# Performance work log

Measured on AMD Instinct MI355X. Metric: run time of the kernel, lower is better.

Reference implementation:

```python
import jax, jax.numpy as jnp
import numpy as np

B, S, D = 2, 1024, 2048
MLP_RATIO = 4
N_LAYERS = 2
H = D * MLP_RATIO
EPS = 1e-5


def _act_quant(x):
    # BitNet b1.58: per-token int8 absmax quantization over last dim
    scale = 127.0 / jnp.clip(jnp.max(jnp.abs(x), axis=-1, keepdims=True), EPS, None)
    return jnp.clip(jnp.round(x * scale), -128.0, 127.0) / scale


def _weight_quant(w):
    # BitNet b1.58: per-tensor ternary quantization with mean-abs scale
    scale = 1.0 / jnp.clip(jnp.mean(jnp.abs(w)), EPS, None)
    return jnp.clip(jnp.round(w * scale), -1.0, 1.0) / scale


def _ste(v, quant_fn):
    # straight-through estimator: forward quantized, backward identity
    return v + jax.lax.stop_gradient(quant_fn(v) - v)


def bit_linear(x, w, b):
    # x: [B,S,in], w: [out,in], b: [out]
    xq = _ste(x, _act_quant)
    wq = _ste(w, _weight_quant)
    return jnp.einsum('bsi,oi->bso', xq, wq) + b


def setup_inputs() -> dict:
    key = jax.random.key(0)
    ks = jax.random.split(key, 16)
    inp = {
        'x': jax.random.normal(ks[0], (B, S, D), jnp.float32),
        'y': jax.random.normal(ks[1], (B, S, D), jnp.float32),
        'z': jax.random.normal(ks[2], (B, S, D), jnp.float32),
        'focus_mask': jax.random.uniform(ks[3], (B, S, 1), jnp.float32),
        'w_in': jax.random.normal(ks[4], (D, 3 * D), jnp.float32) * 0.02,
        'b_in': jnp.zeros((D,), jnp.float32),
        'fc1_w': jax.random.normal(ks[5], (N_LAYERS, H, D), jnp.float32) * 0.02,
        'fc1_b': jnp.zeros((N_LAYERS, H), jnp.float32),
        'fc2_w': jax.random.normal(ks[6], (N_LAYERS, D, H), jnp.float32) * 0.02,
        'fc2_b': jnp.zeros((N_LAYERS, D), jnp.float32),
        'w_out': jax.random.normal(ks[7], (D, D), jnp.float32) * 0.02,
        'b_out': jnp.zeros((D,), jnp.float32),
    }
    return inp


def reference(x, y, z, focus_mask, w_in, b_in, fc1_w, fc1_b, fc2_w, fc2_b, w_out, b_out):
    h = bit_linear(jnp.concatenate([x, y, z], axis=-1), w_in, b_in)
    for l in range(N_LAYERS):
        u = jax.nn.gelu(bit_linear(h, fc1_w[l], fc1_b[l]), approximate=False)
        h = h + bit_linear(u, fc2_w[l], fc2_b[l])
    delta = bit_linear(h, w_out, b_out)
    return y + focus_mask * delta
```

## Files before the change

### kernel.cpp

```cpp
#include <hip/hip_runtime.h>

#define EPSQ 1e-5f

typedef int i32x4 __attribute__((ext_vector_type(4)));
typedef float f32x4n __attribute__((ext_vector_type(4)));

__device__ __forceinline__ unsigned short f2bf(float f) {
  unsigned int b = __builtin_bit_cast(unsigned int, f);
  b += 0x7FFFu + ((b >> 16) & 1u);
  return (unsigned short)(b >> 16);
}
__device__ __forceinline__ float bf2f(unsigned short u) {
  unsigned int b = ((unsigned int)u) << 16;
  return __builtin_bit_cast(float, b);
}
__device__ __forceinline__ int packw4(float a, float b, float c, float d, float inv) {
  int qa = (int)fminf(fmaxf(rintf(a * inv), -1.0f), 1.0f);
  int qb = (int)fminf(fmaxf(rintf(b * inv), -1.0f), 1.0f);
  int qc = (int)fminf(fmaxf(rintf(c * inv), -1.0f), 1.0f);
  int qd = (int)fminf(fmaxf(rintf(d * inv), -1.0f), 1.0f);
  return (qa & 255) | ((qb & 255) << 8) | ((qc & 255) << 16) | ((qd & 255) << 24);
}
__device__ __forceinline__ int packa4(float a, float b, float c, float d, float s) {
  int qa = (int)fminf(fmaxf(rintf(a * s), -128.0f), 127.0f);
  int qb = (int)fminf(fmaxf(rintf(b * s), -128.0f), 127.0f);
  int qc = (int)fminf(fmaxf(rintf(c * s), -128.0f), 127.0f);
  int qd = (int)fminf(fmaxf(rintf(d * s), -128.0f), 127.0f);
  return (qa & 255) | ((qb & 255) << 8) | ((qc & 255) << 16) | ((qd & 255) << 24);
}

struct WTbl {
  const float* p[6];
  unsigned char* q[6];
  unsigned int cum[7];
};

__global__ __launch_bounds__(256) void wmean_partial(WTbl tbl, double* __restrict__ part) {
  const int b = blockIdx.x;
  int t = 0;
#pragma unroll
  for (int i = 1; i < 6; ++i) t += (b >= (int)tbl.cum[i]);
  const f32x4n* __restrict__ p = (const f32x4n*)tbl.p[t];
  const unsigned int base = (unsigned)(b - (int)tbl.cum[t]) * 2048u + threadIdx.x;
  f32x4n v[8];
#pragma unroll
  for (int u = 0; u < 8; ++u) v[u] = __builtin_nontemporal_load(p + base + (unsigned)u * 256u);
  double s = 0.0;
#pragma unroll
  for (int u = 0; u < 8; ++u)
    s += (double)(fabsf(v[u][0]) + fabsf(v[u][1])) + (double)(fabsf(v[u][2]) + fabsf(v[u][3]));
  for (int off = 32; off; off >>= 1) s += __shfl_xor(s, off);
  __shared__ double wsum[4];
  if ((threadIdx.x & 63) == 0) wsum[threadIdx.x >> 6] = s;
  __syncthreads();
  if (threadIdx.x == 0) part[b] = (wsum[0] + wsum[1]) + (wsum[2] + wsum[3]);
}

__global__ __launch_bounds__(256) void wmean_final(const double* __restrict__ part,
                                                   WTbl tbl, float* wmean) {
  for (int t = 0; t < 6; ++t) {
    const int lo = (int)tbl.cum[t], hi = (int)tbl.cum[t + 1];
    double s = 0.0;
    for (int i = lo + (int)threadIdx.x; i < hi; i += 256) s += part[i];
    for (int off = 32; off; off >>= 1) s += __shfl_xor(s, off);
    __shared__ double w4[4];
    if ((threadIdx.x & 63) == 0) w4[threadIdx.x >> 6] = s;
    __syncthreads();
    if (threadIdx.x == 0) {
      const double n = (double)(hi - lo) * 8192.0;
      float m = (float)(((w4[0] + w4[1]) + (w4[2] + w4[3])) / n);
      if (m < EPSQ) m = EPSQ;
      wmean[t] = m;
    }
    __syncthreads();
  }
}

__global__ __launch_bounds__(256) void wquant(WTbl tbl, const float* wmean) {
  const int b = blockIdx.x;
  int t = 0;
#pragma unroll
  for (int i = 1; i < 6; ++i) t += (b >= (int)tbl.cum[i]);
  const float inv = 1.0f / wmean[t];
  const f32x4n* __restrict__ p = (const f32x4n*)tbl.p[t];
  int* __restrict__ q = (int*)tbl.q[t];
  const unsigned int base = (unsigned)(b - (int)tbl.cum[t]) * 2048u + threadIdx.x;
  f32x4n v[8];
#pragma unroll
  for (int u = 0; u < 8; ++u) v[u] = __builtin_nontemporal_load(p + base + (unsigned)u * 256u);
#pragma unroll
  for (int u = 0; u < 8; ++u)
    q[base + (unsigned)u * 256u] = packw4(v[u][0], v[u][1], v[u][2], v[u][3], inv);
}

__device__ __forceinline__ float block_max256(float m) {
  for (int off = 32; off; off >>= 1) m = fmaxf(m, __shfl_xor(m, off));
  __shared__ float wm[4];
  if ((threadIdx.x & 63) == 0) wm[threadIdx.x >> 6] = m;
  __syncthreads();
  return fmaxf(fmaxf(wm[0], wm[1]), fmaxf(wm[2], wm[3]));
}

__global__ __launch_bounds__(256) void aq_cat(const float* x, const float* y, const float* z,
                                              unsigned char* q, float* rsx) {
  const int row = blockIdx.x, tid = threadIdx.x;
  const float4* px = (const float4*)(x + (size_t)row * 2048);
  const float4* py = (const float4*)(y + (size_t)row * 2048);
  const float4* pz = (const float4*)(z + (size_t)row * 2048);
  float4 v[6];
  v[0] = px[tid]; v[1] = px[tid + 256];
  v[2] = py[tid]; v[3] = py[tid + 256];
  v[4] = pz[tid]; v[5] = pz[tid + 256];
  float m = 0.0f;
#pragma unroll
  for (int k = 0; k < 6; ++k)
    m = fmaxf(m, fmaxf(fmaxf(fabsf(v[k].x), fabsf(v[k].y)), fmaxf(fabsf(v[k].z), fabsf(v[k].w))));
  m = fmaxf(block_max256(m), EPSQ);
  const float s = 127.0f / m;
  if (tid == 0) rsx[row] = m / 127.0f;
  int* qr = (int*)(q + (size_t)row * 6144);
#pragma unroll
  for (int k = 0; k < 6; ++k) qr[k * 256 + tid] = packa4(v[k].x, v[k].y, v[k].z, v[k].w, s);
}

__global__ __launch_bounds__(256) void aq_bf16(const unsigned short* u, unsigned char* q, float* rsx) {
  const int row = blockIdx.x, tid = threadIdx.x;
  const uint4* pu = (const uint4*)(u + (size_t)row * 8192);
  float f[32];
#pragma unroll
  for (int k = 0; k < 4; ++k) {
    uint4 w = pu[tid + 256 * k];
    unsigned int ws4[4] = {w.x, w.y, w.z, w.w};
#pragma unroll
    for (int j = 0; j < 4; ++j) {
      f[k * 8 + j * 2 + 0] = bf2f((unsigned short)(ws4[j] & 0xFFFFu));
      f[k * 8 + j * 2 + 1] = bf2f((unsigned short)(ws4[j] >> 16));
    }
  }
  float m = 0.0f;
#pragma unroll
  for (int k = 0; k < 32; ++k) m = fmaxf(m, fabsf(f[k]));
  m = fmaxf(block_max256(m), EPSQ);
  const float s = 127.0f / m;
  if (tid == 0) rsx[row] = m / 127.0f;
  int* qp = (int*)(q + (size_t)row * 8192);
#pragma unroll
  for (int k = 0; k < 4; ++k) {
    qp[(tid + 256 * k) * 2 + 0] = packa4(f[k * 8 + 0], f[k * 8 + 1], f[k * 8 + 2], f[k * 8 + 3], s);
    qp[(tid + 256 * k) * 2 + 1] = packa4(f[k * 8 + 4], f[k * 8 + 5], f[k * 8 + 6], f[k * 8 + 7], s);
  }
}

template<int EPI>
__global__ __launch_bounds__(256) void gemm_bt(
    const unsigned char* __restrict__ A,
    const unsigned char* __restrict__ Bw,
    const float* rsx, const float* wmean, const float* bias,
    float* outF, unsigned short* outB, int* outI,
    int M, int N, int K, int Ksz) {
  __shared__ unsigned char As[2][128 * 128];
  __shared__ unsigned char Bs[2][128 * 128];
  const int tid = threadIdx.x;

  const int gx = gridDim.x, gy = gridDim.y;
  const int orig = blockIdx.y * gx + blockIdx.x;
  const int xcd = orig & 7;
  const int local = orig >> 3;
  const int cn = (gx >= 32) ? 8 : 4;
  const int npx = gx / cn;
  const int n = (xcd % cn) * npx + (local % npx);
  const int m = (xcd / cn) * (gy / (8 / cn)) + (local / npx);
  const int brow = m << 7;
  const int bcol = n << 7;

  const int lane = tid & 63;
  const int wv = tid >> 6;
  const int wr = (wv >> 1) << 6;
  const int wc = (wv & 1) << 6;
  const int lr = lane & 15;
  const int lg = lane >> 4;

  i32x4 acc[4][4] = {};

  const int scol = (((tid & 7) ^ ((tid >> 3) & 7)) << 4);
  const size_t koff = (size_t)blockIdx.z * Ksz;
  const unsigned char* gA0 = A + (size_t)(brow + (tid >> 3)) * K + koff + scol;
  const unsigned char* gB0 = Bw + (size_t)(bcol + (tid >> 3)) * K + koff + scol;
  const int ldst = (tid & ~63) * 16;

  auto stage = [&](int b, int kt) {
#pragma unroll
    for (int c = 0; c < 4; ++c) {
      __builtin_amdgcn_global_load_lds(
          (const __attribute__((address_space(1))) void*)(gA0 + (size_t)kt * 128 + (size_t)c * 32 * K),
          (__attribute__((address_space(3))) void*)(&As[b][c * 4096 + ldst]),
          16, 0, 0);
      __builtin_amdgcn_global_load_lds(
          (const __attribute__((address_space(1))) void*)(gB0 + (size_t)kt * 128 + (size_t)c * 32 * K),
          (__attribute__((address_space(3))) void*)(&Bs[b][c * 4096 + ldst]),
          16, 0, 0);
    }
  };

  const int nkt = Ksz >> 7;
  stage(0, 0);
  stage(1, 1);

  for (int kt = 0; kt < nkt; ++kt) {
    const int cur = kt & 1;
    if (kt + 1 < nkt) {
      asm volatile("s_waitcnt vmcnt(8)" ::: "memory");
    } else {
      asm volatile("s_waitcnt vmcnt(0)" ::: "memory");
    }
    __builtin_amdgcn_s_barrier();
    __builtin_amdgcn_sched_barrier(0);
    __builtin_amdgcn_s_setprio(1);
#pragma unroll
    for (int kk = 0; kk < 2; ++kk) {
      i32x4 af[4], bfr[4];
#pragma unroll
      for (int i = 0; i < 4; ++i) {
        const int ra = wr + i * 16 + lr;
        const int rb = wc + i * 16 + lr;
        const int ch = (((kk << 2) | lg) ^ (lr & 7)) << 4;
        af[i]  = *(const i32x4*)(&As[cur][ra * 128 + ch]);
        bfr[i] = *(const i32x4*)(&Bs[cur][rb * 128 + ch]);
      }
#pragma unroll
      for (int i = 0; i < 4; ++i)
#pragma unroll
        for (int j = 0; j < 4; ++j)
          acc[i][j] = __builtin_amdgcn_mfma_i32_16x16x64_i8(af[i], bfr[j], acc[i][j], 0, 0, 0);
    }
    __builtin_amdgcn_s_setprio(0);
    __builtin_amdgcn_sched_barrier(0);
    __builtin_amdgcn_s_barrier();
    __builtin_amdgcn_sched_barrier(0);
    if (kt + 2 < nkt) stage(cur, kt + 2);
  }

  const float mscale = (EPI == 4) ? 0.0f : wmean[0];
  int* pI = (EPI == 4) ? (outI + (size_t)blockIdx.z * M * N) : nullptr;
#pragma unroll
  for (int i = 0; i < 4; ++i) {
#pragma unroll
    for (int r = 0; r < 4; ++r) {
      const int row = brow + wr + i * 16 + lg * 4 + r;
      const float sc = (EPI == 4) ? 1.0f : rsx[row] * mscale;
#pragma unroll
      for (int j = 0; j < 4; ++j) {
        const int col = bcol + wc + j * 16 + lr;
        const size_t o = (size_t)row * N + col;
        if constexpr (EPI == 4) {
          pI[o] = acc[i][j][r];
        } else {
          float v = (float)acc[i][j][r] * sc + bias[col];
          float g = 0.5f * v * (1.0f + erff(v * 0.70710678118654752f));
          outB[o] = f2bf(g);
        }
      }
    }
  }
}

template<int EPI, bool WRITE_H>
__global__ __launch_bounds__(256) void reduce_qa(
    const int* __restrict__ part, int S, size_t MN,
    const float* __restrict__ wmean, const float* __restrict__ bias,
    float* __restrict__ hbuf, float* __restrict__ rsx,
    unsigned char* __restrict__ qa) {
  const int row = blockIdx.x, tid = threadIdx.x;
  const float sc = rsx[row] * wmean[0];
  const size_t rbase = (size_t)row * 2048;
  int4 v0 = *(const int4*)(part + rbase + (size_t)tid * 4);
  int4 v1 = *(const int4*)(part + rbase + (size_t)(tid + 256) * 4);
  for (int s = 1; s < S; ++s) {
    const int* ps = part + (size_t)s * MN + rbase;
    int4 a0 = *(const int4*)(ps + (size_t)tid * 4);
    int4 a1 = *(const int4*)(ps + (size_t)(tid + 256) * 4);
    v0.x += a0.x; v0.y += a0.y; v0.z += a0.z; v0.w += a0.w;
    v1.x += a1.x; v1.y += a1.y; v1.z += a1.z; v1.w += a1.w;
  }
  const float4 b0 = *(const float4*)(bias + tid * 4);
  const float4 b1 = *(const float4*)(bias + (tid + 256) * 4);
  float4 r0, r1;
  r0.x = (float)v0.x * sc + b0.x; r0.y = (float)v0.y * sc + b0.y;
  r0.z = (float)v0.z * sc + b0.z; r0.w = (float)v0.w * sc + b0.w;
  r1.x = (float)v1.x * sc + b1.x; r1.y = (float)v1.y * sc + b1.y;
  r1.z = (float)v1.z * sc + b1.z; r1.w = (float)v1.w * sc + b1.w;
  if constexpr (EPI == 2) {
    const float4 h0 = *(const float4*)(hbuf + rbase + (size_t)tid * 4);
    const float4 h1 = *(const float4*)(hbuf + rbase + (size_t)(tid + 256) * 4);
    r0.x += h0.x; r0.y += h0.y; r0.z += h0.z; r0.w += h0.w;
    r1.x += h1.x; r1.y += h1.y; r1.z += h1.z; r1.w += h1.w;
  }
  float m = fmaxf(fmaxf(fmaxf(fabsf(r0.x), fabsf(r0.y)), fmaxf(fabsf(r0.z), fabsf(r0.w))),
                  fmaxf(fmaxf(fabsf(r1.x), fabsf(r1.y)), fmaxf(fabsf(r1.z), fabsf(r1.w))));
  m = fmaxf(block_max256(m), EPSQ);
  const float s127 = 127.0f / m;
  if (tid == 0) rsx[row] = m / 127.0f;
  if constexpr (WRITE_H) {
    *(float4*)(hbuf + rbase + (size_t)tid * 4) = r0;
    *(float4*)(hbuf + rbase + (size_t)(tid + 256) * 4) = r1;
  }
  int* qp = (int*)(qa + rbase);
  qp[tid]       = packa4(r0.x, r0.y, r0.z, r0.w, s127);
  qp[tid + 256] = packa4(r1.x, r1.y, r1.z, r1.w, s127);
}

__global__ __launch_bounds__(256) void reduce_final(
    const int* __restrict__ part, int S, int N, size_t MN,
    const float* rsx, const float* wmean, const float* bias,
    const float* aux, const float* focus, float* outF) {
  const size_t i4 = ((size_t)blockIdx.x * 256 + threadIdx.x) * 4;
  if (i4 >= MN) return;
  const int row = (int)(i4 / (unsigned)N);
  const int col = (int)(i4 % (unsigned)N);
  int4 v = *(const int4*)(part + i4);
  for (int s = 1; s < S; ++s) {
    int4 p = *(const int4*)(part + (size_t)s * MN + i4);
    v.x += p.x; v.y += p.y; v.z += p.z; v.w += p.w;
  }
  const float sc = rsx[row] * wmean[0];
  const float4 b = *(const float4*)(bias + col);
  const float4 a = *(const float4*)(aux + i4);
  const float fm = focus[row];
  float4 r;
  r.x = a.x + fm * ((float)v.x * sc + b.x);
  r.y = a.y + fm * ((float)v.y * sc + b.y);
  r.z = a.z + fm * ((float)v.z * sc + b.z);
  r.w = a.w + fm * ((float)v.w * sc + b.w);
  *(float4*)(outF + i4) = r;
}

extern "C" void kernel_launch(void* const* d_in, const int* in_sizes, int n_in,
                              void* d_out, int out_size, void* d_ws, size_t ws_size,
                              hipStream_t stream) {
  const float* x     = (const float*)d_in[0];
  const float* y     = (const float*)d_in[1];
  const float* z     = (const float*)d_in[2];
  const float* fmsk  = (const float*)d_in[3];
  const float* w_in  = (const float*)d_in[4];
  const float* b_in  = (const float*)d_in[5];
  const float* fc1_w = (const float*)d_in[6];
  const float* fc1_b = (const float*)d_in[7];
  const float* fc2_w = (const float*)d_in[8];
  const float* fc2_b = (const float*)d_in[9];
  const float* w_out = (const float*)d_in[10];
  const float* b_out = (const float*)d_in[11];
  float* out = (float*)d_out;

  const int M = 2048;
  const int D = 2048, H = 8192, K3 = 6144;
  const size_t MN = (size_t)M * D;

  char* ws = (char*)d_ws;
  size_t off = 0;
  auto alloc = [&](size_t bytes) { size_t r = off; off = (off + bytes + 255) & ~(size_t)255; return r; };
  unsigned char* wq_in   = (unsigned char*)(ws + alloc((size_t)D * K3));
  unsigned char* wq_fc10 = (unsigned char*)(ws + alloc((size_t)H * D));
  unsigned char* wq_fc11 = (unsigned char*)(ws + alloc((size_t)H * D));
  unsigned char* wq_fc20 = (unsigned char*)(ws + alloc((size_t)D * H));
  unsigned char* wq_fc21 = (unsigned char*)(ws + alloc((size_t)D * H));
  unsigned char* wq_out  = (unsigned char*)(ws + alloc((size_t)D * D));
  unsigned char* qact    = (unsigned char*)(ws + alloc((size_t)M * H));
  unsigned short* ub     = (unsigned short*)(ws + alloc((size_t)M * H * 2));
  float* hbuf            = (float*)(ws + alloc(MN * 4));
  float* rsx             = (float*)(ws + alloc((size_t)M * 4));
  float* wmean           = (float*)(ws + alloc(64));
  double* part           = (double*)(ws + alloc(16384 * 8));
  int* pacc              = (int*)(ws + alloc(MN * 2 * 4));
  (void)in_sizes; (void)n_in; (void)out_size; (void)ws_size;

  WTbl tbl;
  tbl.p[0] = w_in;                  tbl.q[0] = wq_in;
  tbl.p[1] = fc1_w;                 tbl.q[1] = wq_fc10;
  tbl.p[2] = fc1_w + (size_t)H * D; tbl.q[2] = wq_fc11;
  tbl.p[3] = fc2_w;                 tbl.q[3] = wq_fc20;
  tbl.p[4] = fc2_w + (size_t)D * H; tbl.q[4] = wq_fc21;
  tbl.p[5] = w_out;                 tbl.q[5] = wq_out;
  tbl.cum[0] = 0;
  tbl.cum[1] = 1536;
  tbl.cum[2] = 1536 + 2048;
  tbl.cum[3] = 1536 + 2 * 2048;
  tbl.cum[4] = 1536 + 3 * 2048;
  tbl.cum[5] = 1536 + 4 * 2048;
  tbl.cum[6] = 1536 + 4 * 2048 + 512;

  dim3 blk(256);
  const int NCH = 10240;
  wmean_partial<<<dim3(NCH), blk, 0, stream>>>(tbl, part);
  wmean_final<<<dim3(1), blk, 0, stream>>>(part, tbl, wmean);
  wquant<<<dim3(NCH), blk, 0, stream>>>(tbl, wmean);

  aq_cat<<<dim3(M), blk, 0, stream>>>(x, y, z, qact, rsx);
  gemm_bt<4><<<dim3(D / 128, M / 128, 2), blk, 0, stream>>>(qact, wq_in, rsx, wmean + 0, b_in,
                                                            nullptr, nullptr, pacc, M, D, K3, K3 / 2);
  reduce_qa<0, true><<<dim3(M), blk, 0, stream>>>(pacc, 2, MN, wmean + 0, b_in,
                                                  hbuf, rsx, qact);

  unsigned char* wq_fc1[2] = {wq_fc10, wq_fc11};
  unsigned char* wq_fc2[2] = {wq_fc20, wq_fc21};
  for (int l = 0; l < 2; ++l) {
    gemm_bt<1><<<dim3(H / 128, M / 128), blk, 0, stream>>>(qact, wq_fc1[l], rsx, wmean + 1 + l,
                                                           fc1_b + (size_t)l * H,
                                                           nullptr, ub, nullptr, M, H, D, D);
    aq_bf16<<<dim3(M), blk, 0, stream>>>(ub, qact, rsx);
    gemm_bt<4><<<dim3(D / 128, M / 128, 2), blk, 0, stream>>>(qact, wq_fc2[l], rsx, wmean + 3 + l,
                                                              fc2_b + (size_t)l * D,
                                                              nullptr, nullptr, pacc, M, D, H, H / 2);
    if (l == 0) {
      reduce_qa<2, true><<<dim3(M), blk, 0, stream>>>(pacc, 2, MN, wmean + 3 + l,
                                                      fc2_b + (size_t)l * D, hbuf, rsx, qact);
    } else {
      reduce_qa<2, false><<<dim3(M), blk, 0, stream>>>(pacc, 2, MN, wmean + 3 + l,
                                                       fc2_b + (size_t)l * D, hbuf, rsx, qact);
    }
  }

  gemm_bt<4><<<dim3(D / 128, M / 128, 2), blk, 0, stream>>>(qact, wq_out, rsx, wmean + 5, b_out,
                                                            nullptr, nullptr, pacc, M, D, D, D / 2);
  reduce_final<<<dim3((int)((MN / 4 + 255) / 256)), blk, 0, stream>>>(pacc, 2, D, MN, rsx, wmean + 5, b_out,
                                                                      y, fmsk, out);
}
```

Before: 444.6 us.

## Use 256x256-tile 512-thread int8 GEMM kernel for fc1 layers

Adds a dedicated fc1 GEMM kernel with 256x256 output tiles, 8 waves per block each computing a 128x64 sub-tile, and double-buffered direct-to-LDS loads. Larger tiles raise arithmetic intensity and cut global/LDS traffic per MFMA for the largest GEMMs. In exchange it uses 128KB of LDS and many accumulator registers, which limits occupancy, and the grid shrinks to 32x8 blocks.

```diff
diff --git a/kernel.cpp b/kernel.cpp
--- a/kernel.cpp
+++ b/kernel.cpp
@@ -153,8 +153,7 @@
 
 template<int EPI>
 __global__ __launch_bounds__(256) void gemm_bt(
-    const unsigned char* __restrict__ A,
-    const unsigned char* __restrict__ Bw,
+    const unsigned char* __restrict__ A, const unsigned char* __restrict__ Bw,
     const float* rsx, const float* wmean, const float* bias,
     float* outF, unsigned short* outB, int* outI,
     int M, int N, int K, int Ksz) {
@@ -259,6 +258,109 @@
           float g = 0.5f * v * (1.0f + erff(v * 0.70710678118654752f));
           outB[o] = f2bf(g);
         }
+      }
+    }
+  }
+}
+
+__global__ __launch_bounds__(512, 2) void gemm_fc1(
+    const unsigned char* __restrict__ A,
+    const unsigned char* __restrict__ Bw,
+    const float* rsx, const float* wmean, const float* bias,
+    unsigned short* outB, int M, int N, int K) {
+  __shared__ unsigned char As[2][256 * 128];
+  __shared__ unsigned char Bs[2][256 * 128];
+  const int tid = threadIdx.x;
+
+  const int gx = gridDim.x, gy = gridDim.y;
+  const int orig = blockIdx.y * gx + blockIdx.x;
+  const int xcd = orig & 7;
+  const int local = orig >> 3;
+  const int cn = (gx >= 32) ? 8 : 4;
+  const int npx = gx / cn;
+  const int n = (xcd % cn) * npx + (local % npx);
+  const int m = (xcd / cn) * (gy / (8 / cn)) + (local / npx);
+  const int brow = m << 8;
+  const int bcol = n << 8;
+
+  const int lane = tid & 63;
+  const int wv = tid >> 6;
+  const int wr = (wv >> 2) << 7;
+  const int wc = (wv & 3) << 6;
+  const int lr = lane & 15;
+  const int lg = lane >> 4;
+
+  i32x4 acc[8][4] = {};
+
+  const int scol = (((tid & 7) ^ ((tid >> 3) & 7)) << 4);
+  const unsigned char* gA0 = A + (size_t)(brow + (tid >> 3)) * K + scol;
+  const unsigned char* gB0 = Bw + (size_t)(bcol + (tid >> 3)) * K + scol;
+  const int ldst = (tid & ~63) * 16;
+
+  auto stage = [&](int b, int kt) {
+#pragma unroll
+    for (int c = 0; c < 4; ++c) {
+      __builtin_amdgcn_global_load_lds(
+          (const __attribute__((address_space(1))) void*)(gA0 + (size_t)kt * 128 + (size_t)c * 64 * K),
+          (__attribute__((address_space(3))) void*)(&As[b][c * 8192 + ldst]),
+          16, 0, 0);
+      __builtin_amdgcn_global_load_lds(
+          (const __attribute__((address_space(1))) void*)(gB0 + (size_t)kt * 128 + (size_t)c * 64 * K),
+          (__attribute__((address_space(3))) void*)(&Bs[b][c * 8192 + ldst]),
+          16, 0, 0);
+    }
+  };
+
+  const int nkt = K >> 7;
+  stage(0, 0);
+  stage(1, 1);
+
+  for (int kt = 0; kt < nkt; ++kt) {
+    const int cur = kt & 1;
+    if (kt + 1 < nkt) {
+      asm volatile("s_waitcnt vmcnt(8)" ::: "memory");
+    } else {
+      asm volatile("s_waitcnt vmcnt(0)" ::: "memory");
+    }
+    __builtin_amdgcn_s_barrier();
+    __builtin_amdgcn_sched_barrier(0);
+    __builtin_amdgcn_s_setprio(1);
+#pragma unroll
+    for (int kk = 0; kk < 2; ++kk) {
+      const int ch = (((kk << 2) | lg) ^ (lr & 7)) << 4;
+      i32x4 af[8], bfr[4];
+#pragma unroll
+      for (int i = 0; i < 8; ++i)
+        af[i] = *(const i32x4*)(&As[cur][(wr + i * 16 + lr) * 128 + ch]);
+#pragma unroll
+      for (int j = 0; j < 4; ++j)
+        bfr[j] = *(const i32x4*)(&Bs[cur][(wc + j * 16 + lr) * 128 + ch]);
+#pragma unroll
+      for (int i = 0; i < 8; ++i)
+#pragma unroll
+        for (int j = 0; j < 4; ++j)
+          acc[i][j] = __builtin_amdgcn_mfma_i32_16x16x64_i8(af[i], bfr[j], acc[i][j], 0, 0, 0);
+    }
+    __builtin_amdgcn_s_setprio(0);
+    __builtin_amdgcn_sched_barrier(0);
+    __builtin_amdgcn_s_barrier();
+    __builtin_amdgcn_sched_barrier(0);
+    if (kt + 2 < nkt) stage(cur, kt + 2);
+  }
+
+  const float mscale = wmean[0];
+#pragma unroll
+  for (int i = 0; i < 8; ++i) {
+#pragma unroll
+    for (int r = 0; r < 4; ++r) {
+      const int row = brow + wr + i * 16 + lg * 4 + r;
+      const float sc = rsx[row] * mscale;
+#pragma unroll
+      for (int j = 0; j < 4; ++j) {
+        const int col = bcol + wc + j * 16 + lr;
+        float v = (float)acc[i][j][r] * sc + bias[col];
+        float g = 0.5f * v * (1.0f + erff(v * 0.70710678118654752f));
+        outB[(size_t)row * N + col] = f2bf(g);
       }
     }
   }
@@ -403,9 +505,8 @@
   unsigned char* wq_fc1[2] = {wq_fc10, wq_fc11};
   unsigned char* wq_fc2[2] = {wq_fc20, wq_fc21};
   for (int l = 0; l < 2; ++l) {
-    gemm_bt<1><<<dim3(H / 128, M / 128), blk, 0, stream>>>(qact, wq_fc1[l], rsx, wmean + 1 + l,
-                                                           fc1_b + (size_t)l * H,
-                                                           nullptr, ub, nullptr, M, H, D, D);
+    gemm_fc1<<<dim3(H / 256, M / 256), dim3(512), 0, stream>>>(qact, wq_fc1[l], rsx, wmean + 1 + l,
+                                                               fc1_b + (size_t)l * H, ub, M, H, D);
     aq_bf16<<<dim3(M), blk, 0, stream>>>(ub, qact, rsx);
     gemm_bt<4><<<dim3(D / 128, M / 128, 2), blk, 0, stream>>>(qact, wq_fc2[l], rsx, wmean + 3 + l,
                                                               fc2_b + (size_t)l * D,
```

New measurement: 437.4 us (median of 3 runs). About the same (-1.6%).
